# Performance work log

Measured on AMD Instinct MI355X. Metric: run time of the kernel, lower is better.

## Reference

```python
import jax, jax.numpy as jnp
import numpy as np

B, H, W, C = 16, 64, 64, 256


def setup_inputs() -> dict:
    key = jax.random.key(0)
    k1, k2, k3 = jax.random.split(key, 3)
    x = jax.random.normal(k1, (B, H, W, C), dtype=jnp.float32)
    # 1x1 convs are channel matmuls; lecun_normal ~ N(0, 1/fan_in)
    W_qkv = jax.random.normal(k2, (C, 3 * C), dtype=jnp.float32) / np.sqrt(C)
    W_out = jax.random.normal(k3, (C, C), dtype=jnp.float32) / np.sqrt(C)
    b_out = jnp.zeros((C,), dtype=jnp.float32)
    return {"x": x, "W_qkv": W_qkv, "W_out": W_out, "b_out": b_out}


def reference(x, W_qkv, W_out, b_out):
    b, h, w, c = x.shape
    n = h * w
    # to_qkv: 1x1 conv, no bias -> channel matmul
    qkv = jnp.einsum('bhwc,cd->bhwd', x, W_qkv)            # [b,h,w,3c]
    q, k, v = jnp.split(qkv, 3, axis=-1)                    # each [b,h,w,c]
    # rearrange to [b, c, n] (heads=1)
    q = q.reshape(b, n, c).transpose(0, 2, 1)
    k = k.reshape(b, n, c).transpose(0, 2, 1)
    v = v.reshape(b, n, c).transpose(0, 2, 1)
    k = jax.nn.softmax(k, axis=-1)                          # softmax over spatial n
    context = jnp.einsum('bdn,ben->bde', k, v)              # [b,c,c] per-sample context
    out = jnp.einsum('bde,bdn->ben', context, q)            # [b,c,n]
    out = out.reshape(b, c, h, w).transpose(0, 2, 3, 1)     # [b,h,w,c]
    # to_out: 1x1 conv with bias
    return jnp.einsum('bhwc,cd->bhwd', out, W_out) + b_out
```

## Files before the change

### kernel.cpp

```cpp
#include <hip/hip_runtime.h>
#include <hip/hip_bf16.h>


typedef __bf16 bf16;
typedef __bf16 bf16x4 __attribute__((ext_vector_type(4)));
typedef __bf16 bf16x8 __attribute__((ext_vector_type(8)));
typedef float  f32x4  __attribute__((ext_vector_type(4)));

#define LDP 72

__device__ __forceinline__ bf16 tob(float f) { return (bf16)f; }

__device__ __forceinline__ void compute_tile(const bf16* As, const bf16* Bs,
                                             f32x4 acc[4][4], int wr, int wc,
                                             int lr, int g) {
#pragma unroll
  for (int ks = 0; ks < 2; ++ks) {
    bf16x8 a[4], b[4];
#pragma unroll
    for (int m = 0; m < 4; ++m)
      a[m] = *reinterpret_cast<const bf16x8*>(&As[(wr * 64 + m * 16 + lr) * LDP + ks * 32 + g * 8]);
#pragma unroll
    for (int n = 0; n < 4; ++n)
      b[n] = *reinterpret_cast<const bf16x8*>(&Bs[(wc * 64 + n * 16 + lr) * LDP + ks * 32 + g * 8]);
#pragma unroll
    for (int m = 0; m < 4; ++m)
#pragma unroll
      for (int n = 0; n < 4; ++n)
        acc[m][n] = __builtin_amdgcn_mfma_f32_16x16x32_bf16(a[m], b[n], acc[m][n], 0, 0, 0);
  }
}

__global__ __launch_bounds__(256) void k_wt(const float* __restrict__ Wq,
                                            const float* __restrict__ Wo,
                                            bf16* __restrict__ WqT,
                                            bf16* __restrict__ WoT,
                                            float* __restrict__ S) {
  int idx = blockIdx.x * 256 + threadIdx.x;
  if (idx < 196608) {
    int n = idx >> 8, k = idx & 255;
    WqT[idx] = tob(Wq[(size_t)k * 768 + n]);
  } else {
    int i2 = idx - 196608;
    int co = i2 >> 8, e = i2 & 255;
    WoT[i2] = tob(Wo[(size_t)e * 256 + co]);
  }
  if (idx < 4096) S[idx] = 0.0f;
}

__global__ __launch_bounds__(256) void k_qkv(const float* __restrict__ x,
                                             const bf16* __restrict__ WqT,
                                             bf16* __restrict__ Q,
                                             bf16* __restrict__ Et,
                                             bf16* __restrict__ Vt,
                                             float* __restrict__ S) {
  __shared__ __align__(16) bf16 As[128 * LDP];
  __shared__ __align__(16) bf16 Bs[128 * LDP];
  int bx = blockIdx.x;
  int rb = bx / 6, cb = bx % 6;
  int tid = threadIdx.x;
  int lane = tid & 63, w = tid >> 6;
  int wr = w >> 1, wc = w & 1;
  int g = lane >> 4, lr = lane & 15;
  const int rowbase = rb * 128, colbase = cb * 128;

  f32x4 acc[4][4];
#pragma unroll
  for (int m = 0; m < 4; ++m)
#pragma unroll
    for (int n = 0; n < 4; ++n) acc[m][n] = (f32x4)0.0f;

  for (int kt = 0; kt < 4; ++kt) {
    int k0 = kt * 64;
    __syncthreads();
#pragma unroll
    for (int r = 0; r < 8; ++r) {
      int idx = r * 1024 + tid * 4;
      int row = idx >> 6, col = idx & 63;
      float4 v = *reinterpret_cast<const float4*>(x + (size_t)(rowbase + row) * 256 + k0 + col);
      bf16x4 p;
      p[0] = tob(v.x); p[1] = tob(v.y); p[2] = tob(v.z); p[3] = tob(v.w);
      *reinterpret_cast<bf16x4*>(&As[row * LDP + col]) = p;
    }
#pragma unroll
    for (int r = 0; r < 4; ++r) {
      int idx = r * 2048 + tid * 8;
      int row = idx >> 6, col = idx & 63;
      bf16x8 v = *reinterpret_cast<const bf16x8*>(WqT + (size_t)(colbase + row) * 256 + k0 + col);
      *reinterpret_cast<bf16x8*>(&Bs[row * LDP + col]) = v;
    }
    __syncthreads();
    compute_tile(As, Bs, acc, wr, wc, lr, g);
  }

  int grow = rowbase + wr * 64;
  int gcol = colbase + wc * 64;
  int sec = gcol >> 8;
  int coff = gcol & 255;
  int b = grow >> 12;
  int nsp = grow & 4095;

  if (sec == 0) {
#pragma unroll
    for (int m = 0; m < 4; ++m)
#pragma unroll
      for (int n = 0; n < 4; ++n) {
        int col = coff + n * 16 + lr;
#pragma unroll
        for (int t = 0; t < 4; ++t) {
          int row = grow + m * 16 + g * 4 + t;
          Q[(size_t)row * 256 + col] = tob(acc[m][n][t]);
        }
      }
  } else {
    bf16* dst = (sec == 1) ? Et : Vt;
    float cs0 = 0.f, cs1 = 0.f, cs2 = 0.f, cs3 = 0.f;
#pragma unroll
    for (int m = 0; m < 4; ++m)
#pragma unroll
      for (int n = 0; n < 4; ++n) {
        int col = coff + n * 16 + lr;
        int nn0 = nsp + m * 16 + g * 4;
        bf16x4 p;
#pragma unroll
        for (int t = 0; t < 4; ++t) {
          float v = acc[m][n][t];
          if (sec == 1) {
            v = expf(v);
            if (n == 0) cs0 += v; else if (n == 1) cs1 += v;
            else if (n == 2) cs2 += v; else cs3 += v;
          }
          p[t] = tob(v);
        }
        *reinterpret_cast<bf16x4*>(&dst[((size_t)(b * 256 + col) << 12) + nn0]) = p;
      }
    if (sec == 1) {
      cs0 += __shfl_xor(cs0, 16); cs0 += __shfl_xor(cs0, 32);
      cs1 += __shfl_xor(cs1, 16); cs1 += __shfl_xor(cs1, 32);
      cs2 += __shfl_xor(cs2, 16); cs2 += __shfl_xor(cs2, 32);
      cs3 += __shfl_xor(cs3, 16); cs3 += __shfl_xor(cs3, 32);
      float v = (g == 0) ? cs0 : (g == 1) ? cs1 : (g == 2) ? cs2 : cs3;
      atomicAdd(&S[b * 256 + coff + g * 16 + lr], v);
    }
  }
}

__global__ __launch_bounds__(256) void k_ctx(const bf16* __restrict__ Et,
                                             const bf16* __restrict__ Vt,
                                             float* __restrict__ part) {
  __shared__ __align__(16) bf16 As[128 * LDP];
  __shared__ __align__(16) bf16 Bs[128 * LDP];
  int bx = blockIdx.x;
  int tile = bx & 3, dblk = tile >> 1, eblk = tile & 1;
  int s = (bx >> 2) & 3;
  int b = bx >> 4;
  int tid = threadIdx.x;
  int lane = tid & 63, w = tid >> 6;
  int wr = w >> 1, wc = w & 1;
  int g = lane >> 4, lr = lane & 15;

  const bf16* Ab = Et + ((size_t)(b * 256 + dblk * 128) << 12);
  const bf16* Bb = Vt + ((size_t)(b * 256 + eblk * 128) << 12);
  int n0 = s * 1024;

  f32x4 acc[4][4];
#pragma unroll
  for (int m = 0; m < 4; ++m)
#pragma unroll
    for (int n = 0; n < 4; ++n) acc[m][n] = (f32x4)0.0f;

  for (int kt = 0; kt < 16; ++kt) {
    int k0 = n0 + kt * 64;
    __syncthreads();
#pragma unroll
    for (int r = 0; r < 4; ++r) {
      int idx = r * 2048 + tid * 8;
      int row = idx >> 6, col = idx & 63;
      bf16x8 va = *reinterpret_cast<const bf16x8*>(Ab + (size_t)row * 4096 + k0 + col);
      *reinterpret_cast<bf16x8*>(&As[row * LDP + col]) = va;
      bf16x8 vb = *reinterpret_cast<const bf16x8*>(Bb + (size_t)row * 4096 + k0 + col);
      *reinterpret_cast<bf16x8*>(&Bs[row * LDP + col]) = vb;
    }
    __syncthreads();
    compute_tile(As, Bs, acc, wr, wc, lr, g);
  }

  float* p = part + (size_t)(b * 4 + s) * 65536;
  int dbase = dblk * 128 + wr * 64;
  int ebase = eblk * 128 + wc * 64;
#pragma unroll
  for (int m = 0; m < 4; ++m)
#pragma unroll
    for (int n = 0; n < 4; ++n)
#pragma unroll
      for (int t = 0; t < 4; ++t)
        p[(size_t)(dbase + m * 16 + g * 4 + t) * 256 + ebase + n * 16 + lr] = acc[m][n][t];
}

__global__ __launch_bounds__(256) void k_wc(const float* __restrict__ part,
                                            const float* __restrict__ S,
                                            const bf16* __restrict__ WoT,
                                            bf16* __restrict__ WcT) {
  __shared__ __align__(16) bf16 As[128 * LDP];
  __shared__ __align__(16) bf16 Bs[128 * LDP];
  int bx = blockIdx.x;
  int b = bx >> 2, dblk = (bx >> 1) & 1, cblk = bx & 1;
  int tid = threadIdx.x;
  int lane = tid & 63, w = tid >> 6;
  int wr = w >> 1, wc = w & 1;
  int g = lane >> 4, lr = lane & 15;
  const float* p0 = part + (size_t)b * 4 * 65536;

  f32x4 acc[4][4];
#pragma unroll
  for (int m = 0; m < 4; ++m)
#pragma unroll
    for (int n = 0; n < 4; ++n) acc[m][n] = (f32x4)0.0f;

  for (int kt = 0; kt < 4; ++kt) {
    int k0 = kt * 64;
    __syncthreads();
#pragma unroll
    for (int r = 0; r < 8; ++r) {
      int idx = r * 1024 + tid * 4;
      int row = idx >> 6, col = idx & 63;
      int d = dblk * 128 + row;
      size_t off = (size_t)d * 256 + k0 + col;
      float4 v0 = *reinterpret_cast<const float4*>(p0 + off);
      float4 v1 = *reinterpret_cast<const float4*>(p0 + 65536 + off);
      float4 v2 = *reinterpret_cast<const float4*>(p0 + 2 * 65536 + off);
      float4 v3 = *reinterpret_cast<const float4*>(p0 + 3 * 65536 + off);
      float rs = 1.0f / S[b * 256 + d];
      bf16x4 p;
      p[0] = tob((v0.x + v1.x + v2.x + v3.x) * rs);
      p[1] = tob((v0.y + v1.y + v2.y + v3.y) * rs);
      p[2] = tob((v0.z + v1.z + v2.z + v3.z) * rs);
      p[3] = tob((v0.w + v1.w + v2.w + v3.w) * rs);
      *reinterpret_cast<bf16x4*>(&As[row * LDP + col]) = p;
    }
#pragma unroll
    for (int r = 0; r < 4; ++r) {
      int idx = r * 2048 + tid * 8;
      int row = idx >> 6, col = idx & 63;
      bf16x8 v = *reinterpret_cast<const bf16x8*>(WoT + (size_t)(cblk * 128 + row) * 256 + k0 + col);
      *reinterpret_cast<bf16x8*>(&Bs[row * LDP + col]) = v;
    }
    __syncthreads();
    compute_tile(As, Bs, acc, wr, wc, lr, g);
  }

  int dbase = dblk * 128 + wr * 64;
  int cbase = cblk * 128 + wc * 64;
#pragma unroll
  for (int m = 0; m < 4; ++m)
#pragma unroll
    for (int n = 0; n < 4; ++n) {
      int co = cbase + n * 16 + lr;
      int d0 = dbase + m * 16 + g * 4;
      bf16x4 p;
#pragma unroll
      for (int t = 0; t < 4; ++t) p[t] = tob(acc[m][n][t]);
      *reinterpret_cast<bf16x4*>(&WcT[(size_t)b * 65536 + (size_t)co * 256 + d0]) = p;
    }
}

__global__ __launch_bounds__(256) void k_out(const bf16* __restrict__ Q,
                                             const bf16* __restrict__ WcT,
                                             const float* __restrict__ b_out,
                                             float* __restrict__ y) {
  __shared__ __align__(16) bf16 As[128 * LDP];
  __shared__ __align__(16) bf16 Bs[128 * LDP];
  int bx = blockIdx.x;
  int rb = bx >> 1, cbk = bx & 1;
  int tid = threadIdx.x;
  int lane = tid & 63, w = tid >> 6;
  int wr = w >> 1, wc = w & 1;
  int g = lane >> 4, lr = lane & 15;
  int rowbase = rb * 128;
  int b = rowbase >> 12;
  const bf16* Bb = WcT + (size_t)b * 65536;

  f32x4 acc[4][4];
#pragma unroll
  for (int m = 0; m < 4; ++m)
#pragma unroll
    for (int n = 0; n < 4; ++n) acc[m][n] = (f32x4)0.0f;

  for (int kt = 0; kt < 4; ++kt) {
    int k0 = kt * 64;
    __syncthreads();
#pragma unroll
    for (int r = 0; r < 4; ++r) {
      int idx = r * 2048 + tid * 8;
      int row = idx >> 6, col = idx & 63;
      bf16x8 va = *reinterpret_cast<const bf16x8*>(Q + (size_t)(rowbase + row) * 256 + k0 + col);
      *reinterpret_cast<bf16x8*>(&As[row * LDP + col]) = va;
      bf16x8 vb = *reinterpret_cast<const bf16x8*>(Bb + (size_t)(cbk * 128 + row) * 256 + k0 + col);
      *reinterpret_cast<bf16x8*>(&Bs[row * LDP + col]) = vb;
    }
    __syncthreads();
    compute_tile(As, Bs, acc, wr, wc, lr, g);
  }

  int cbase = cbk * 128 + wc * 64;
#pragma unroll
  for (int m = 0; m < 4; ++m)
#pragma unroll
    for (int n = 0; n < 4; ++n) {
      int col = cbase + n * 16 + lr;
      float bo = b_out[col];
#pragma unroll
      for (int t = 0; t < 4; ++t) {
        int row = rowbase + wr * 64 + m * 16 + g * 4 + t;
        y[(size_t)row * 256 + col] = acc[m][n][t] + bo;
      }
    }
}

extern "C" void kernel_launch(void* const* d_in, const int* in_sizes, int n_in,
                              void* d_out, int out_size, void* d_ws, size_t ws_size,
                              hipStream_t stream) {
  (void)in_sizes; (void)n_in; (void)out_size; (void)ws_size;
  const float* x  = (const float*)d_in[0];
  const float* Wq = (const float*)d_in[1];
  const float* Wo = (const float*)d_in[2];
  const float* bo = (const float*)d_in[3];
  float* y = (float*)d_out;

  char* ws = (char*)d_ws;
  bf16*  Q    = (bf16*)(ws);
  bf16*  Et   = (bf16*)(ws + 33554432);
  bf16*  Vt   = (bf16*)(ws + 67108864);
  float* part = (float*)(ws + 100663296);
  bf16*  WcT  = (bf16*)(ws + 117440512);
  bf16*  WqT  = (bf16*)(ws + 119537664);
  bf16*  WoT  = (bf16*)(ws + 119930880);
  float* S    = (float*)(ws + 120061952);

  k_wt<<<dim3(1024), dim3(256), 0, stream>>>(Wq, Wo, WqT, WoT, S);
  k_qkv<<<dim3(3072), dim3(256), 0, stream>>>(x, WqT, Q, Et, Vt, S);
  k_ctx<<<dim3(256), dim3(256), 0, stream>>>(Et, Vt, part);
  k_wc<<<dim3(64), dim3(256), 0, stream>>>(part, S, WoT, WcT);
  k_out<<<dim3(1024), dim3(256), 0, stream>>>(Q, WcT, bo, y);
}
```

Measured before the change: 262.1 us.

## Stage GEMM tiles with global_load_lds, pre-convert x to bf16, swizzle blocks

Adds a prep kernel that converts x to bf16 once, so the QKV GEMM can stage both operands straight into LDS with global_load_lds instead of going through registers. The LDS tiles drop their padding to a dense 64-wide layout, which may bring back bank conflicts on the MFMA operand reads. Block indices in the qkv, ctx and out kernels are swizzled to improve cache locality. The ctx reduction is split 8 ways instead of 4, giving more blocks for parallelism at the cost of more partial sums for k_wc to add up.

```diff
diff --git a/kernel.cpp b/kernel.cpp
--- a/kernel.cpp
+++ b/kernel.cpp
@@ -11,14 +11,50 @@
 
 __device__ __forceinline__ bf16 tob(float f) { return (bf16)f; }
 
-__device__ __forceinline__ void compute_tile(const bf16* As, const bf16* Bs,
-                                             f32x4 acc[4][4], int wr, int wc,
-                                             int lr, int g) {
+__device__ __forceinline__ void gl_lds16(const void* g, void* l) {
+  __builtin_amdgcn_global_load_lds(
+      (const __attribute__((address_space(1))) void*)g,
+      (__attribute__((address_space(3))) void*)l, 16, 0, 0);
+}
+
+__device__ __forceinline__ void stage128x64(const bf16* __restrict__ src,
+                                            size_t stride, bf16* lds, int tid) {
+#pragma unroll
+  for (int r = 0; r < 4; ++r) {
+    int e = (r * 256 + tid) * 8;
+    int row = e >> 6, col = e & 63;
+    gl_lds16(src + (size_t)row * stride + col, lds + e);
+  }
+}
+
+__device__ __forceinline__ void compute_tile64(const bf16* As, const bf16* Bs,
+                                               f32x4 acc[4][4], int wr, int wc,
+                                               int lr, int g) {
 #pragma unroll
   for (int ks = 0; ks < 2; ++ks) {
     bf16x8 a[4], b[4];
 #pragma unroll
     for (int m = 0; m < 4; ++m)
+      a[m] = *reinterpret_cast<const bf16x8*>(&As[(wr * 64 + m * 16 + lr) * 64 + ks * 32 + g * 8]);
+#pragma unroll
+    for (int n = 0; n < 4; ++n)
+      b[n] = *reinterpret_cast<const bf16x8*>(&Bs[(wc * 64 + n * 16 + lr) * 64 + ks * 32 + g * 8]);
+#pragma unroll
+    for (int m = 0; m < 4; ++m)
+#pragma unroll
+      for (int n = 0; n < 4; ++n)
+        acc[m][n] = __builtin_amdgcn_mfma_f32_16x16x32_bf16(a[m], b[n], acc[m][n], 0, 0, 0);
+  }
+}
+
+__device__ __forceinline__ void compute_tileP(const bf16* As, const bf16* Bs,
+                                              f32x4 acc[4][4], int wr, int wc,
+                                              int lr, int g) {
+#pragma unroll
+  for (int ks = 0; ks < 2; ++ks) {
+    bf16x8 a[4], b[4];
+#pragma unroll
+    for (int m = 0; m < 4; ++m)
       a[m] = *reinterpret_cast<const bf16x8*>(&As[(wr * 64 + m * 16 + lr) * LDP + ks * 32 + g * 8]);
 #pragma unroll
     for (int n = 0; n < 4; ++n)
@@ -31,33 +67,53 @@
   }
 }
 
-__global__ __launch_bounds__(256) void k_wt(const float* __restrict__ Wq,
-                                            const float* __restrict__ Wo,
-                                            bf16* __restrict__ WqT,
-                                            bf16* __restrict__ WoT,
-                                            float* __restrict__ S) {
-  int idx = blockIdx.x * 256 + threadIdx.x;
-  if (idx < 196608) {
-    int n = idx >> 8, k = idx & 255;
-    WqT[idx] = tob(Wq[(size_t)k * 768 + n]);
+__global__ __launch_bounds__(256) void k_prep(const float* __restrict__ x,
+                                              const float* __restrict__ Wq,
+                                              const float* __restrict__ Wo,
+                                              bf16* __restrict__ xb,
+                                              bf16* __restrict__ WqT,
+                                              bf16* __restrict__ WoT,
+                                              float* __restrict__ S) {
+  int b = blockIdx.x, tid = threadIdx.x;
+  if (b < 4096) {
+    size_t base = (size_t)b * 4096;
+#pragma unroll
+    for (int r = 0; r < 4; ++r) {
+      size_t e = base + r * 1024 + tid * 4;
+      float4 v = *reinterpret_cast<const float4*>(x + e);
+      bf16x4 p;
+      p[0] = tob(v.x); p[1] = tob(v.y); p[2] = tob(v.z); p[3] = tob(v.w);
+      *reinterpret_cast<bf16x4*>(xb + e) = p;
+    }
+    if (b < 16) S[b * 256 + tid] = 0.0f;
   } else {
-    int i2 = idx - 196608;
-    int co = i2 >> 8, e = i2 & 255;
-    WoT[i2] = tob(Wo[(size_t)e * 256 + co]);
-  }
-  if (idx < 4096) S[idx] = 0.0f;
-}
-
-__global__ __launch_bounds__(256) void k_qkv(const float* __restrict__ x,
+    int i0 = (b - 4096) * 1024 + tid * 4;
+#pragma unroll
+    for (int j = 0; j < 4; ++j) {
+      int idx = i0 + j;
+      if (idx < 196608) {
+        int n = idx >> 8, k = idx & 255;
+        WqT[idx] = tob(Wq[(size_t)k * 768 + n]);
+      } else {
+        int i2 = idx - 196608;
+        int co = i2 >> 8, e2 = i2 & 255;
+        WoT[i2] = tob(Wo[(size_t)e2 * 256 + co]);
+      }
+    }
+  }
+}
+
+__global__ __launch_bounds__(256) void k_qkv(const bf16* __restrict__ xb,
                                              const bf16* __restrict__ WqT,
                                              bf16* __restrict__ Q,
                                              bf16* __restrict__ Et,
                                              bf16* __restrict__ Vt,
                                              float* __restrict__ S) {
-  __shared__ __align__(16) bf16 As[128 * LDP];
-  __shared__ __align__(16) bf16 Bs[128 * LDP];
+  __shared__ __align__(16) bf16 As[128 * 64];
+  __shared__ __align__(16) bf16 Bs[128 * 64];
   int bx = blockIdx.x;
-  int rb = bx / 6, cb = bx % 6;
+  int swz = (bx & 7) * 384 + (bx >> 3);
+  int rb = swz / 6, cb = swz % 6;
   int tid = threadIdx.x;
   int lane = tid & 63, w = tid >> 6;
   int wr = w >> 1, wc = w & 1;
@@ -73,24 +129,10 @@
   for (int kt = 0; kt < 4; ++kt) {
     int k0 = kt * 64;
     __syncthreads();
-#pragma unroll
-    for (int r = 0; r < 8; ++r) {
-      int idx = r * 1024 + tid * 4;
-      int row = idx >> 6, col = idx & 63;
-      float4 v = *reinterpret_cast<const float4*>(x + (size_t)(rowbase + row) * 256 + k0 + col);
-      bf16x4 p;
-      p[0] = tob(v.x); p[1] = tob(v.y); p[2] = tob(v.z); p[3] = tob(v.w);
-      *reinterpret_cast<bf16x4*>(&As[row * LDP + col]) = p;
-    }
-#pragma unroll
-    for (int r = 0; r < 4; ++r) {
-      int idx = r * 2048 + tid * 8;
-      int row = idx >> 6, col = idx & 63;
-      bf16x8 v = *reinterpret_cast<const bf16x8*>(WqT + (size_t)(colbase + row) * 256 + k0 + col);
-      *reinterpret_cast<bf16x8*>(&Bs[row * LDP + col]) = v;
-    }
-    __syncthreads();
-    compute_tile(As, Bs, acc, wr, wc, lr, g);
+    stage128x64(xb + (size_t)rowbase * 256 + k0, 256, As, tid);
+    stage128x64(WqT + (size_t)colbase * 256 + k0, 256, Bs, tid);
+    __syncthreads();
+    compute_tile64(As, Bs, acc, wr, wc, lr, g);
   }
 
   int grow = rowbase + wr * 64;
@@ -148,20 +190,20 @@
 __global__ __launch_bounds__(256) void k_ctx(const bf16* __restrict__ Et,
                                              const bf16* __restrict__ Vt,
                                              float* __restrict__ part) {
-  __shared__ __align__(16) bf16 As[128 * LDP];
-  __shared__ __align__(16) bf16 Bs[128 * LDP];
+  __shared__ __align__(16) bf16 As[128 * 64];
+  __shared__ __align__(16) bf16 Bs[128 * 64];
   int bx = blockIdx.x;
-  int tile = bx & 3, dblk = tile >> 1, eblk = tile & 1;
-  int s = (bx >> 2) & 3;
-  int b = bx >> 4;
+  int swz = (bx & 7) * 64 + (bx >> 3);
+  int tile = swz & 3, dblk = tile >> 1, eblk = tile & 1;
+  int s = (swz >> 2) & 7;
+  int b = swz >> 5;
   int tid = threadIdx.x;
   int lane = tid & 63, w = tid >> 6;
   int wr = w >> 1, wc = w & 1;
   int g = lane >> 4, lr = lane & 15;
 
-  const bf16* Ab = Et + ((size_t)(b * 256 + dblk * 128) << 12);
-  const bf16* Bb = Vt + ((size_t)(b * 256 + eblk * 128) << 12);
-  int n0 = s * 1024;
+  const bf16* Ab = Et + (((size_t)(b * 256 + dblk * 128)) << 12) + s * 512;
+  const bf16* Bb = Vt + (((size_t)(b * 256 + eblk * 128)) << 12) + s * 512;
 
   f32x4 acc[4][4];
 #pragma unroll
@@ -169,23 +211,15 @@
 #pragma unroll
     for (int n = 0; n < 4; ++n) acc[m][n] = (f32x4)0.0f;
 
-  for (int kt = 0; kt < 16; ++kt) {
-    int k0 = n0 + kt * 64;
-    __syncthreads();
-#pragma unroll
-    for (int r = 0; r < 4; ++r) {
-      int idx = r * 2048 + tid * 8;
-      int row = idx >> 6, col = idx & 63;
-      bf16x8 va = *reinterpret_cast<const bf16x8*>(Ab + (size_t)row * 4096 + k0 + col);
-      *reinterpret_cast<bf16x8*>(&As[row * LDP + col]) = va;
-      bf16x8 vb = *reinterpret_cast<const bf16x8*>(Bb + (size_t)row * 4096 + k0 + col);
-      *reinterpret_cast<bf16x8*>(&Bs[row * LDP + col]) = vb;
-    }
-    __syncthreads();
-    compute_tile(As, Bs, acc, wr, wc, lr, g);
-  }
-
-  float* p = part + (size_t)(b * 4 + s) * 65536;
+  for (int kt = 0; kt < 8; ++kt) {
+    __syncthreads();
+    stage128x64(Ab + kt * 64, 4096, As, tid);
+    stage128x64(Bb + kt * 64, 4096, Bs, tid);
+    __syncthreads();
+    compute_tile64(As, Bs, acc, wr, wc, lr, g);
+  }
+
+  float* p = part + (size_t)(b * 8 + s) * 65536;
   int dbase = dblk * 128 + wr * 64;
   int ebase = eblk * 128 + wc * 64;
 #pragma unroll
@@ -209,7 +243,7 @@
   int lane = tid & 63, w = tid >> 6;
   int wr = w >> 1, wc = w & 1;
   int g = lane >> 4, lr = lane & 15;
-  const float* p0 = part + (size_t)b * 4 * 65536;
+  const float* p0 = part + (size_t)b * 8 * 65536;
 
   f32x4 acc[4][4];
 #pragma unroll
@@ -226,16 +260,20 @@
       int row = idx >> 6, col = idx & 63;
       int d = dblk * 128 + row;
       size_t off = (size_t)d * 256 + k0 + col;
-      float4 v0 = *reinterpret_cast<const float4*>(p0 + off);
-      float4 v1 = *reinterpret_cast<const float4*>(p0 + 65536 + off);
-      float4 v2 = *reinterpret_cast<const float4*>(p0 + 2 * 65536 + off);
-      float4 v3 = *reinterpret_cast<const float4*>(p0 + 3 * 65536 + off);
+      float4 a0 = *reinterpret_cast<const float4*>(p0 + off);
+      float4 a1 = *reinterpret_cast<const float4*>(p0 + 65536 + off);
+      float4 a2 = *reinterpret_cast<const float4*>(p0 + 2 * 65536 + off);
+      float4 a3 = *reinterpret_cast<const float4*>(p0 + 3 * 65536 + off);
+      float4 a4 = *reinterpret_cast<const float4*>(p0 + 4 * 65536 + off);
+      float4 a5 = *reinterpret_cast<const float4*>(p0 + 5 * 65536 + off);
+      float4 a6 = *reinterpret_cast<const float4*>(p0 + 6 * 65536 + off);
+      float4 a7 = *reinterpret_cast<const float4*>(p0 + 7 * 65536 + off);
       float rs = 1.0f / S[b * 256 + d];
       bf16x4 p;
-      p[0] = tob((v0.x + v1.x + v2.x + v3.x) * rs);
-      p[1] = tob((v0.y + v1.y + v2.y + v3.y) * rs);
-      p[2] = tob((v0.z + v1.z + v2.z + v3.z) * rs);
-      p[3] = tob((v0.w + v1.w + v2.w + v3.w) * rs);
+      p[0] = tob((a0.x + a1.x + a2.x + a3.x + a4.x + a5.x + a6.x + a7.x) * rs);
+      p[1] = tob((a0.y + a1.y + a2.y + a3.y + a4.y + a5.y + a6.y + a7.y) * rs);
+      p[2] = tob((a0.z + a1.z + a2.z + a3.z + a4.z + a5.z + a6.z + a7.z) * rs);
+      p[3] = tob((a0.w + a1.w + a2.w + a3.w + a4.w + a5.w + a6.w + a7.w) * rs);
       *reinterpret_cast<bf16x4*>(&As[row * LDP + col]) = p;
     }
 #pragma unroll
@@ -246,7 +284,7 @@
       *reinterpret_cast<bf16x8*>(&Bs[row * LDP + col]) = v;
     }
     __syncthreads();
-    compute_tile(As, Bs, acc, wr, wc, lr, g);
+    compute_tileP(As, Bs, acc, wr, wc, lr, g);
   }
 
   int dbase = dblk * 128 + wr * 64;
@@ -268,10 +306,11 @@
                                              const bf16* __restrict__ WcT,
                                              const float* __restrict__ b_out,
                                              float* __restrict__ y) {
-  __shared__ __align__(16) bf16 As[128 * LDP];
-  __shared__ __align__(16) bf16 Bs[128 * LDP];
+  __shared__ __align__(16) bf16 As[128 * 64];
+  __shared__ __align__(16) bf16 Bs[128 * 64];
   int bx = blockIdx.x;
-  int rb = bx >> 1, cbk = bx & 1;
+  int swz = (bx & 7) * 128 + (bx >> 3);
+  int rb = swz >> 1, cbk = swz & 1;
   int tid = threadIdx.x;
   int lane = tid & 63, w = tid >> 6;
   int wr = w >> 1, wc = w & 1;
@@ -289,17 +328,10 @@
   for (int kt = 0; kt < 4; ++kt) {
     int k0 = kt * 64;
     __syncthreads();
-#pragma unroll
-    for (int r = 0; r < 4; ++r) {
-      int idx = r * 2048 + tid * 8;
-      int row = idx >> 6, col = idx & 63;
-      bf16x8 va = *reinterpret_cast<const bf16x8*>(Q + (size_t)(rowbase + row) * 256 + k0 + col);
-      *reinterpret_cast<bf16x8*>(&As[row * LDP + col]) = va;
-      bf16x8 vb = *reinterpret_cast<const bf16x8*>(Bb + (size_t)(cbk * 128 + row) * 256 + k0 + col);
-      *reinterpret_cast<bf16x8*>(&Bs[row * LDP + col]) = vb;
-    }
-    __syncthreads();
-    compute_tile(As, Bs, acc, wr, wc, lr, g);
+    stage128x64(Q + (size_t)rowbase * 256 + k0, 256, As, tid);
+    stage128x64(Bb + (size_t)(cbk * 128) * 256 + k0, 256, Bs, tid);
+    __syncthreads();
+    compute_tile64(As, Bs, acc, wr, wc, lr, g);
   }
 
   int cbase = cbk * 128 + wc * 64;
@@ -331,15 +363,16 @@
   bf16*  Q    = (bf16*)(ws);
   bf16*  Et   = (bf16*)(ws + 33554432);
   bf16*  Vt   = (bf16*)(ws + 67108864);
+  bf16*  xb   = (bf16*)(ws + 100663296);
   float* part = (float*)(ws + 100663296);
-  bf16*  WcT  = (bf16*)(ws + 117440512);
-  bf16*  WqT  = (bf16*)(ws + 119537664);
-  bf16*  WoT  = (bf16*)(ws + 119930880);
-  float* S    = (float*)(ws + 120061952);
-
-  k_wt<<<dim3(1024), dim3(256), 0, stream>>>(Wq, Wo, WqT, WoT, S);
-  k_qkv<<<dim3(3072), dim3(256), 0, stream>>>(x, WqT, Q, Et, Vt, S);
-  k_ctx<<<dim3(256), dim3(256), 0, stream>>>(Et, Vt, part);
+  bf16*  WcT  = (bf16*)(ws + 134217728);
+  bf16*  WqT  = (bf16*)(ws + 136314880);
+  bf16*  WoT  = (bf16*)(ws + 136708096);
+  float* S    = (float*)(ws + 136839168);
+
+  k_prep<<<dim3(4352), dim3(256), 0, stream>>>(x, Wq, Wo, xb, WqT, WoT, S);
+  k_qkv<<<dim3(3072), dim3(256), 0, stream>>>(xb, WqT, Q, Et, Vt, S);
+  k_ctx<<<dim3(512), dim3(256), 0, stream>>>(Et, Vt, part);
   k_wc<<<dim3(64), dim3(256), 0, stream>>>(part, S, WoT, WcT);
   k_out<<<dim3(1024), dim3(256), 0, stream>>>(Q, WcT, bo, y);
 }
```

Measured after the change: 247.1 us. 1.06x faster.
